# Kernel optimization log

Hardware: AMD Instinct MI355X
Metric: run time of the kernel (lower is better)

Reference implementation:

```python
import jax, jax.numpy as jnp
import numpy as np

K = 12
CHUNK = 1024
N_LAYERS = 4
WIDTH = 192
COND = 64
PE_DIM = 3 * 8 * 2 + 3  # 51
OUT_SCALE = 0.01
BIG = 1e9


def _build_knn(x, k=K, chunk=CHUNK):
    """Brute-force kNN, row-chunked like the TF double-chunked version.
    x: (N,3) float32 -> (N,k) int32 neighbor indices (self excluded)."""
    n = x.shape[0]
    x = x.astype(jnp.float32)
    x_sq = jnp.sum(x * x, axis=1)  # (N,)
    col_ids = jnp.arange(n, dtype=jnp.int32)
    starts = jnp.arange(0, n, chunk, dtype=jnp.int32)

    def one_chunk(start):
        xc = jax.lax.dynamic_slice(x, (start, 0), (chunk, 3))        # (chunk,3)
        sq_c = jax.lax.dynamic_slice(x_sq, (start,), (chunk,))       # (chunk,)
        d = sq_c[:, None] + x_sq[None, :] - 2.0 * (xc @ x.T)         # (chunk,N)
        d = jnp.maximum(d, 0.0)
        rows = start + jnp.arange(chunk, dtype=jnp.int32)
        d = d + jnp.where(rows[:, None] == col_ids[None, :], BIG, 0.0)  # exclude self
        _, idx = jax.lax.top_k(-d, k)                                 # smallest distances
        return idx.astype(jnp.int32)

    idx = jax.lax.map(one_chunk, starts)  # (n/chunk, chunk, k)
    return idx.reshape(n, k)


def _fourier(x, Bs):
    """concat_k [sin(xB_k), cos(xB_k)] + x  -> (N, PE_DIM)."""
    feats = []
    for B in Bs:
        xb = x @ B  # (N,8)
        feats.append(jnp.sin(xb))
        feats.append(jnp.cos(xb))
    feats.append(x)
    return jnp.concatenate(feats, axis=-1)


def setup_inputs() -> dict:
    key = jax.random.key(0)
    ks = jax.random.split(key, 16)
    n = 32768
    x = jax.random.normal(ks[0], (n, 3), dtype=jnp.float32)
    z = jax.random.normal(ks[1], (COND,), dtype=jnp.float32)
    sigmas = (1.0, 10.0, 50.0)
    B0 = jax.random.normal(ks[2], (3, 8), dtype=jnp.float32) * sigmas[0]
    B1 = jax.random.normal(ks[3], (3, 8), dtype=jnp.float32) * sigmas[1]
    B2 = jax.random.normal(ks[4], (3, 8), dtype=jnp.float32) * sigmas[2]
    in_total = PE_DIM + COND  # 115
    s = 0.05
    Wp = jax.random.normal(ks[5], (in_total, WIDTH), dtype=jnp.float32) * s
    bp = jnp.zeros((WIDTH,), dtype=jnp.float32)
    mix_dim = WIDTH + WIDTH + 6  # feat + agg + rel_feat
    Wl = jax.random.normal(ks[6], (N_LAYERS, mix_dim, WIDTH), dtype=jnp.float32) * s
    bl = jnp.zeros((N_LAYERS, WIDTH), dtype=jnp.float32)
    # FiLM: kernel ~zeros, gamma bias=ones, beta bias=zeros (perturbed slightly)
    Wg = jax.random.normal(ks[7], (N_LAYERS, COND, WIDTH), dtype=jnp.float32) * 0.01
    bg = jnp.ones((N_LAYERS, WIDTH), dtype=jnp.float32)
    Wb = jax.random.normal(ks[8], (N_LAYERS, COND, WIDTH), dtype=jnp.float32) * 0.01
    bb = jnp.zeros((N_LAYERS, WIDTH), dtype=jnp.float32)
    Wout = jax.random.normal(ks[9], (WIDTH, 3), dtype=jnp.float32) * s
    bout = jnp.zeros((3,), dtype=jnp.float32)
    return {"x": x, "z": z, "B0": B0, "B1": B1, "B2": B2,
            "Wp": Wp, "bp": bp, "Wl": Wl, "bl": bl,
            "Wg": Wg, "bg": bg, "Wb": Wb, "bb": bb,
            "Wout": Wout, "bout": bout}


def reference(x, z, B0, B1, B2, Wp, bp, Wl, bl, Wg, bg, Wb, bb, Wout, bout):
    n = x.shape[0]
    knn_idx = _build_knn(x)                     # (N,K) int32
    pe = _fourier(x, (B0, B1, B2))              # (N,51)
    zb = jnp.broadcast_to(z[None, :], (n, COND))
    feat = jnp.concatenate([pe, zb], axis=-1)   # (N,115)
    h = jax.nn.silu(feat @ Wp + bp)             # (N,WIDTH)
    # precompute relative-coordinate stats (same for all layers)
    nbr_coords = x[knn_idx]                     # (N,K,3)
    rel = nbr_coords - x[:, None, :]
    rel_feat = jnp.concatenate([rel.mean(axis=1), rel.std(axis=1)], axis=-1)  # (N,6)
    for li in range(N_LAYERS):
        nbr = h[knn_idx]                        # (N,K,WIDTH) gather
        agg = nbr.mean(axis=1)                  # (N,WIDTH)
        mix = jnp.concatenate([h, agg, rel_feat], axis=-1)  # (N,390)
        h = jax.nn.silu(mix @ Wl[li] + bl[li])
        gamma = z @ Wg[li] + bg[li]             # (WIDTH,)
        beta = z @ Wb[li] + bb[li]
        h = h * gamma[None, :] + beta[None, :]  # FiLM
    out = (h @ Wout + bout) * OUT_SCALE         # (N,3)
    return out
```

## Files before the change

### kernel.cpp

```cpp
#include <hip/hip_runtime.h>
#include <math.h>

#define WIDTH 192
#define KNN 12
#define G 64
#define NCELLS (G * G * G)
#define SMAX 8

#define CE(a, b) { double _lo = fmin(a, b); double _hi = fmax(a, b); a = _lo; b = _hi; }
#define INSERT12(key) { \
    b11 = fmin(b11, key); \
    CE(b10, b11); CE(b9, b10); CE(b8, b9); CE(b7, b8); CE(b6, b7); \
    CE(b5, b6);  CE(b4, b5); CE(b3, b4); CE(b2, b3); CE(b1, b2); CE(b0, b1); }
#define DECL12 double b0,b1,b2,b3,b4,b5,b6,b7,b8,b9,b10,b11
#define INIT12 { b0=__hiloint2double(0x7F7FFFFF,0);  b1=__hiloint2double(0x7F7FFFFF,1); \
    b2=__hiloint2double(0x7F7FFFFF,2);  b3=__hiloint2double(0x7F7FFFFF,3); \
    b4=__hiloint2double(0x7F7FFFFF,4);  b5=__hiloint2double(0x7F7FFFFF,5); \
    b6=__hiloint2double(0x7F7FFFFF,6);  b7=__hiloint2double(0x7F7FFFFF,7); \
    b8=__hiloint2double(0x7F7FFFFF,8);  b9=__hiloint2double(0x7F7FFFFF,9); \
    b10=__hiloint2double(0x7F7FFFFF,10); b11=__hiloint2double(0x7F7FFFFF,11); }

#define MERGE_STAGE(m) { \
    double pb11 = shflx_d(b11, m), pb10 = shflx_d(b10, m), pb9 = shflx_d(b9, m); \
    double pb8  = shflx_d(b8, m),  pb7  = shflx_d(b7, m),  pb6 = shflx_d(b6, m); \
    double pb5  = shflx_d(b5, m),  pb4  = shflx_d(b4, m),  pb3 = shflx_d(b3, m); \
    double pb2  = shflx_d(b2, m),  pb1  = shflx_d(b1, m),  pb0 = shflx_d(b0, m); \
    double c12 = pb3, c13 = pb2, c14 = pb1, c15 = pb0; \
    b4 = fmin(b4, pb11); b5 = fmin(b5, pb10); b6 = fmin(b6, pb9);  b7 = fmin(b7, pb8); \
    b8 = fmin(b8, pb7);  b9 = fmin(b9, pb6);  b10 = fmin(b10, pb5); b11 = fmin(b11, pb4); \
    CE(b0, b8);  CE(b1, b9);  CE(b2, b10); CE(b3, b11); \
    CE(b4, c12); CE(b5, c13); CE(b6, c14); CE(b7, c15); \
    CE(b0, b4);  CE(b1, b5);  CE(b2, b6);  CE(b3, b7); \
    CE(b8, c12); CE(b9, c13); CE(b10, c14); CE(b11, c15); \
    CE(b0, b2);  CE(b1, b3);  CE(b4, b6);  CE(b5, b7); \
    CE(b8, b10); CE(b9, b11); \
    CE(b0, b1);  CE(b2, b3);  CE(b4, b5);  CE(b6, b7); \
    CE(b8, b9);  CE(b10, b11); }

__device__ inline unsigned encf(float f) {
    unsigned u = __float_as_uint(f);
    return (u & 0x80000000u) ? ~u : (u | 0x80000000u);
}
__device__ inline float decf(unsigned u) {
    return (u & 0x80000000u) ? __uint_as_float(u & 0x7fffffffu) : __uint_as_float(~u);
}
__device__ inline int cellc(float v, float mn, float invh) {
    int c = (int)((v - mn) * invh);
    return min(max(c, 0), G - 1);
}
__device__ inline double shflx_d(double v, int m) {
    int lo = __shfl_xor(__double2loint(v), m, 64);
    int hi = __shfl_xor(__double2hiint(v), m, 64);
    return __hiloint2double(hi, lo);
}

__device__ inline float wave_union_d12(
    double b0, double b1, double b2, double b3, double b4, double b5,
    double b6, double b7, double b8, double b9, double b10, double b11)
{
#pragma unroll
    for (int m = 1; m <= 32; m <<= 1) MERGE_STAGE(m)
    return __int_as_float(__double2hiint(b11));
}

__global__ __launch_bounds__(256) void prep_kernel(
    const float4* __restrict__ sorted, const float* __restrict__ B0,
    const float* __restrict__ B1, const float* __restrict__ B2,
    float* __restrict__ pe, int n)
{
    int i = blockIdx.x * 256 + threadIdx.x;
    float4 q = sorted[i];
    float x0 = q.x, x1 = q.y, x2 = q.z;
    const float* Bm[3] = {B0, B1, B2};
    float* pr = pe + (size_t)i * 64;
#pragma unroll
    for (int m = 0; m < 3; ++m) {
        const float* B = Bm[m];
#pragma unroll
        for (int k = 0; k < 8; ++k) {
            float arg = x0 * B[k] + x1 * B[8 + k] + x2 * B[16 + k];
            pr[m * 16 + k]     = sinf(arg);
            pr[m * 16 + 8 + k] = cosf(arg);
        }
    }
    pr[48] = x0; pr[49] = x1; pr[50] = x2;
#pragma unroll
    for (int c = 51; c < 64; ++c) pr[c] = 0.0f;
}

__global__ __launch_bounds__(256) void precompute_kernel(
    const float* __restrict__ z, const float* __restrict__ Wp, const float* __restrict__ bp,
    const float* __restrict__ Wg, const float* __restrict__ bg,
    const float* __restrict__ Wb, const float* __restrict__ bb,
    float* __restrict__ bias0, float* __restrict__ gammaB, float* __restrict__ betaB)
{
    __shared__ float zs[64];
    int t = threadIdx.x;
    if (t < 64) zs[t] = z[t];
    __syncthreads();
    if (t < WIDTH) {
        float acc = bp[t];
        for (int k = 0; k < 64; ++k) acc += zs[k] * Wp[(51 + k) * WIDTH + t];
        bias0[t] = acc;
        for (int l = 0; l < 4; ++l) {
            float g = bg[l * WIDTH + t];
            float b = bb[l * WIDTH + t];
            for (int k = 0; k < 64; ++k) {
                g += zs[k] * Wg[(l * 64 + k) * WIDTH + t];
                b += zs[k] * Wb[(l * 64 + k) * WIDTH + t];
            }
            gammaB[l * WIDTH + t] = g;
            betaB[l * WIDTH + t] = b;
        }
    }
}

__global__ __launch_bounds__(64) void init_bbox_kernel(unsigned* __restrict__ bb)
{
    int t = threadIdx.x;
    if (t < 3) bb[t] = 0xFFFFFFFFu;
    else if (t < 6) bb[t] = 0u;
}

__global__ __launch_bounds__(256) void bbox_kernel(
    const float* __restrict__ x, unsigned* __restrict__ bb, int n)
{
    int i = blockIdx.x * 256 + threadIdx.x;
    unsigned emin[3], emax[3];
#pragma unroll
    for (int a = 0; a < 3; ++a) { unsigned e = encf(x[i * 3 + a]); emin[a] = e; emax[a] = e; }
#pragma unroll
    for (int o = 32; o; o >>= 1) {
#pragma unroll
        for (int a = 0; a < 3; ++a) {
            emin[a] = min(emin[a], (unsigned)__shfl_xor((int)emin[a], o, 64));
            emax[a] = max(emax[a], (unsigned)__shfl_xor((int)emax[a], o, 64));
        }
    }
    if ((threadIdx.x & 63) == 0) {
#pragma unroll
        for (int a = 0; a < 3; ++a) {
            atomicMin(&bb[a], emin[a]);
            atomicMax(&bb[3 + a], emax[a]);
        }
    }
}

__global__ __launch_bounds__(256) void hist_kernel(
    const float* __restrict__ x, const unsigned* __restrict__ bb,
    unsigned* __restrict__ counts, unsigned long long* __restrict__ rowmask, int n)
{
    int i = blockIdx.x * 256 + threadIdx.x;
    float mnx = decf(bb[0]), mny = decf(bb[1]), mnz = decf(bb[2]);
    float ivx = (float)G / (decf(bb[3]) - mnx);
    float ivy = (float)G / (decf(bb[4]) - mny);
    float ivz = (float)G / (decf(bb[5]) - mnz);
    int cx = cellc(x[i * 3 + 0], mnx, ivx);
    int cy = cellc(x[i * 3 + 1], mny, ivy);
    int cz = cellc(x[i * 3 + 2], mnz, ivz);
    atomicAdd(&counts[(cz * G + cy) * G + cx], 1u);
    atomicOr(&rowmask[cz * G + cy], 1ull << cx);
}

__global__ __launch_bounds__(256) void scan1_kernel(
    const unsigned* __restrict__ counts, unsigned* __restrict__ offs,
    unsigned* __restrict__ bsums)
{
    __shared__ unsigned s[256];
    int b = blockIdx.x, t = threadIdx.x;
    unsigned base = (unsigned)b * 1024 + t * 4;
    unsigned v[4], sum = 0;
#pragma unroll
    for (int k = 0; k < 4; ++k) { v[k] = counts[base + k]; sum += v[k]; }
    s[t] = sum; __syncthreads();
    for (int off = 1; off < 256; off <<= 1) {
        unsigned xv = (t >= off) ? s[t - off] : 0u;
        __syncthreads();
        s[t] += xv;
        __syncthreads();
    }
    unsigned excl = s[t] - sum;
    if (t == 255) bsums[b] = s[255];
    unsigned run = excl;
#pragma unroll
    for (int k = 0; k < 4; ++k) { offs[base + k] = run; run += v[k]; }
}

__global__ __launch_bounds__(256) void scan2_kernel(unsigned* __restrict__ bsums)
{
    __shared__ unsigned s[256];
    int t = threadIdx.x;
    unsigned v = bsums[t];
    s[t] = v; __syncthreads();
    for (int off = 1; off < 256; off <<= 1) {
        unsigned xv = (t >= off) ? s[t - off] : 0u;
        __syncthreads();
        s[t] += xv;
        __syncthreads();
    }
    bsums[t] = s[t] - v;
}

__global__ __launch_bounds__(256) void scan3_kernel(
    unsigned* __restrict__ offs, const unsigned* __restrict__ bsums,
    unsigned* __restrict__ cursors, int n)
{
    int b = blockIdx.x, t = threadIdx.x;
    unsigned add = bsums[b];
    unsigned base = (unsigned)b * 1024 + t * 4;
#pragma unroll
    for (int k = 0; k < 4; ++k) {
        unsigned v = offs[base + k] + add;
        offs[base + k] = v;
        cursors[base + k] = v;
    }
    if (b == 255 && t == 255) offs[NCELLS] = (unsigned)n;
}

__global__ __launch_bounds__(256) void scatter_kernel(
    const float* __restrict__ x, const unsigned* __restrict__ bb,
    unsigned* __restrict__ cursors, float4* __restrict__ sorted,
    unsigned* __restrict__ inv, int n)
{
    int i = blockIdx.x * 256 + threadIdx.x;
    float mnx = decf(bb[0]), mny = decf(bb[1]), mnz = decf(bb[2]);
    float ivx = (float)G / (decf(bb[3]) - mnx);
    float ivy = (float)G / (decf(bb[4]) - mny);
    float ivz = (float)G / (decf(bb[5]) - mnz);
    float x0 = x[i * 3 + 0], x1 = x[i * 3 + 1], x2 = x[i * 3 + 2];
    int cx = cellc(x0, mnx, ivx);
    int cy = cellc(x1, mny, ivy);
    int cz = cellc(x2, mnz, ivz);
    unsigned pos = atomicAdd(&cursors[(cz * G + cy) * G + cx], 1u);
    sorted[pos] = make_float4(x0, x1, x2, __int_as_float(i));
    inv[i] = pos;
}

__global__ __launch_bounds__(256) void knn_grid_kernel(
    const float4* __restrict__ sorted, const unsigned* __restrict__ offs,
    const unsigned long long* __restrict__ rowmask,
    const unsigned* __restrict__ bb, const float* __restrict__ x,
    const unsigned* __restrict__ inv,
    unsigned short* __restrict__ knn, float* __restrict__ relf, int n)
{
    const int tid = threadIdx.x;
    const int l = tid & 63;
    const int nb = gridDim.x;
    const int b = blockIdx.x;
    const int fb = (b & 1) ? (nb - 1 - (b >> 1)) : (b >> 1);
    const int p = fb * 4 + (tid >> 6);

    float mnx = decf(bb[0]), mny = decf(bb[1]), mnz = decf(bb[2]);
    float mxx = decf(bb[3]), mxy = decf(bb[4]), mxz = decf(bb[5]);
    float hx = (mxx - mnx) / G, hy = (mxy - mny) / G, hz = (mxz - mnz) / G;
    float ivx = (float)G / (mxx - mnx);
    float ivy = (float)G / (mxy - mny);
    float ivz = (float)G / (mxz - mnz);

    float4 q = sorted[p];
    float xi = q.x, yi = q.y, zi = q.z;
    int iorig = __float_as_int(q.w);
    float sqi = fmaf(zi, zi, fmaf(yi, yi, xi * xi));
    int cx = cellc(xi, mnx, ivx), cy = cellc(yi, mny, ivy), cz = cellc(zi, mnz, ivz);
    float fx = (xi - mnx) - cx * hx;
    float fy = (yi - mny) - cy * hy;
    float fz = (zi - mnz) - cz * hz;

    DECL12; INIT12;
    float worst = 3.402823466e+38f;
    float worst_g = 3.402823466e+38f;

    auto waveMinWorst = [&]() -> float {
        float wm = worst;
        wm = fminf(wm, __shfl_xor(wm, 1, 64));
        wm = fminf(wm, __shfl_xor(wm, 2, 64));
        wm = fminf(wm, __shfl_xor(wm, 4, 64));
        wm = fminf(wm, __shfl_xor(wm, 8, 64));
        wm = fminf(wm, __shfl_xor(wm, 16, 64));
        wm = fminf(wm, __shfl_xor(wm, 32, 64));
        return wm;
    };

    auto lane12Bound = [&]() -> float {
        float v = __int_as_float(__double2hiint(b0));
#pragma unroll
        for (int k = 2; k <= 64; k <<= 1) {
#pragma unroll
            for (int j = k >> 1; j >= 1; j >>= 1) {
                float pv = __shfl_xor(v, j, 64);
                bool dir = ((l & k) == 0);
                bool lower = ((l & j) == 0);
                float mn = fminf(v, pv), mx = fmaxf(v, pv);
                v = (lower == dir) ? mn : mx;
            }
        }
        return __shfl(v, 11, 64);
    };

    auto scanRange = [&](int c0, int c1) {
        unsigned j0 = offs[c0], j1 = offs[c1 + 1];
        if (j0 >= j1) return;
        float4 c = sorted[j0];
        for (unsigned t = j0; t < j1; ++t) {
            unsigned tn = (t + 1 < j1) ? t + 1 : t;
            float4 nx = sorted[tn];
            float sqj = fmaf(c.z, c.z, fmaf(c.y, c.y, c.x * c.x));
            float dot = fmaf(zi, c.z, fmaf(yi, c.y, xi * c.x));
            float d = fmaf(-2.0f, dot, sqi + sqj);
            int jg = __float_as_int(c.w);
            if (d <= fminf(worst, worst_g) && jg != iorig) {
                d = fmaxf(d, 0.0f);
                double key = __hiloint2double(__float_as_int(d), jg);
                INSERT12(key);
                worst = __int_as_float(__double2hiint(b11));
            }
            c = nx;
        }
    };

    bool done = false;
    for (int s = 0; s <= SMAX; ++s) {
        if (s > 0) {
            float bx = (s - 1) * hx + fminf(fx, hx - fx);
            float by = (s - 1) * hy + fminf(fy, hy - fy);
            float bz = (s - 1) * hz + fminf(fz, hz - fz);
            float bnd = fminf(bx, fminf(by, bz));
            float bnd2 = bnd * bnd;
            worst_g = fminf(worst_g, waveMinWorst());
            if (bnd2 > worst_g + 1e-4f) { done = true; break; }
            worst_g = fminf(worst_g, lane12Bound());
            if (bnd2 > worst_g + 1e-4f) { done = true; break; }
            if (s >= 4) {
                worst_g = fminf(worst_g,
                    wave_union_d12(b0,b1,b2,b3,b4,b5,b6,b7,b8,b9,b10,b11));
                if (bnd2 > worst_g + 1e-4f) { done = true; break; }
            }
        }
        if (s == 0) {
            if (l == 0) {
                int row = cz * G + cy;
                if ((rowmask[row] >> cx) & 1ull) {
                    int rb = row * G;
                    scanRange(rb + cx, rb + cx);
                }
            }
        } else {
            int w2 = 2 * s + 1;
            float rcp = 1.0f / (float)w2;
            int nrows = w2 * w2;
            for (int r = l; r < nrows; r += 64) {
                int qd = (int)((float)r * rcp);
                int rem = r - qd * w2;
                if (rem < 0) { qd--; rem += w2; }
                else if (rem >= w2) { qd++; rem -= w2; }
                int dz = qd - s, dy = rem - s;
                int zz = cz + dz, yy = cy + dy;
                if (zz < 0 || zz >= G || yy < 0 || yy >= G) continue;
                int row = zz * G + yy;
                unsigned long long rm = rowmask[row];
                if (rm == 0ull) continue;
                int rb = row * G;
                int adz = dz < 0 ? -dz : dz, ady = dy < 0 ? -dy : dy;
                if (adz == s || ady == s) {
                    int x0 = max(cx - s, 0), x1 = min(cx + s, G - 1);
                    unsigned long long msk =
                        ((x1 == 63) ? ~0ull : ((1ull << (x1 + 1)) - 1ull)) &
                        ~((1ull << x0) - 1ull);
                    unsigned long long mm = rm & msk;
                    if (mm) {
                        int c0 = __ffsll((unsigned long long)mm) - 1;
                        int c1 = 63 - __clzll((long long)mm);
                        scanRange(rb + c0, rb + c1);
                    }
                } else {
                    int xm = cx - s, xp = cx + s;
                    if (xm >= 0 && ((rm >> xm) & 1ull)) scanRange(rb + xm, rb + xm);
                    if (xp < G  && ((rm >> xp) & 1ull)) scanRange(rb + xp, rb + xp);
                }
            }
        }
    }
    if (!done) {
        float bx = SMAX * hx + fminf(fx, hx - fx);
        float by = SMAX * hy + fminf(fy, hy - fy);
        float bz = SMAX * hz + fminf(fz, hz - fz);
        float bnd = fminf(bx, fminf(by, bz));
        float bnd2 = bnd * bnd;
        worst_g = fminf(worst_g, waveMinWorst());
        if (bnd2 > worst_g + 1e-4f) done = true;
        if (!done) {
            worst_g = fminf(worst_g, lane12Bound());
            if (bnd2 > worst_g + 1e-4f) done = true;
        }
        if (!done) {
            worst_g = fminf(worst_g,
                wave_union_d12(b0,b1,b2,b3,b4,b5,b6,b7,b8,b9,b10,b11));
            if (bnd2 > worst_g + 1e-4f) done = true;
        }
    }
    if (!done) {
        INIT12;
        worst = 3.402823466e+38f; worst_g = 3.402823466e+38f;
        for (int base = 0; base < n; base += 512) {
            float4 cc[8];
#pragma unroll
            for (int r = 0; r < 8; ++r) cc[r] = sorted[base + l + r * 64];
#pragma unroll
            for (int r = 0; r < 8; ++r) {
                float4 c = cc[r];
                float sqj = fmaf(c.z, c.z, fmaf(c.y, c.y, c.x * c.x));
                float dot = fmaf(zi, c.z, fmaf(yi, c.y, xi * c.x));
                float d = fmaf(-2.0f, dot, sqi + sqj);
                int jg = __float_as_int(c.w);
                if (d <= fminf(worst, worst_g) && jg != iorig) {
                    d = fmaxf(d, 0.0f);
                    double key = __hiloint2double(__float_as_int(d), jg);
                    INSERT12(key);
                    worst = __int_as_float(__double2hiint(b11));
                }
            }
            worst_g = fminf(worst_g, waveMinWorst());
        }
    }

#pragma unroll
    for (int m = 1; m <= 32; m <<= 1) MERGE_STAGE(m)

    if (l == 0) {
        int idx[KNN];
        idx[0]=__double2loint(b0);  idx[1]=__double2loint(b1);  idx[2]=__double2loint(b2);
        idx[3]=__double2loint(b3);  idx[4]=__double2loint(b4);  idx[5]=__double2loint(b5);
        idx[6]=__double2loint(b6);  idx[7]=__double2loint(b7);  idx[8]=__double2loint(b8);
        idx[9]=__double2loint(b9);  idx[10]=__double2loint(b10); idx[11]=__double2loint(b11);

        float rx[KNN], ry[KNN], rz[KNN];
        float sx = 0.f, sy = 0.f, sz = 0.f;
#pragma unroll
        for (int s = 0; s < KNN; ++s) {
            int j = idx[s];
            knn[(size_t)p * KNN + s] = (unsigned short)inv[j];
            rx[s] = x[(size_t)j * 3 + 0] - xi;
            ry[s] = x[(size_t)j * 3 + 1] - yi;
            rz[s] = x[(size_t)j * 3 + 2] - zi;
            sx += rx[s]; sy += ry[s]; sz += rz[s];
        }
        float mx = sx / 12.0f, my = sy / 12.0f, mz = sz / 12.0f;
        float vx = 0.f, vy = 0.f, vz = 0.f;
#pragma unroll
        for (int s = 0; s < KNN; ++s) {
            float dx = rx[s] - mx, dy = ry[s] - my, dz = rz[s] - mz;
            vx += dx * dx; vy += dy * dy; vz += dz * dz;
        }
        float* rr = relf + (size_t)p * 8;
        rr[0] = mx; rr[1] = my; rr[2] = mz;
        rr[3] = sqrtf(vx / 12.0f); rr[4] = sqrtf(vy / 12.0f); rr[5] = sqrtf(vz / 12.0f);
        rr[6] = 0.0f; rr[7] = 0.0f;
    }
}

template <bool LAYER>
__global__ __launch_bounds__(256) void gemm_silu_kernel(
    const float* __restrict__ A0, const float* __restrict__ Agg,
    const float* __restrict__ Rel,
    const float* __restrict__ W, const float* __restrict__ bias,
    const float* __restrict__ gamma, const float* __restrict__ beta,
    float* __restrict__ out)
{
    __shared__ float As[16][68];
    __shared__ float Bs[16][196];
    const int tid = threadIdx.x;
    const int ty = tid >> 4, tx = tid & 15;
    const int m0 = blockIdx.x * 64;
    const int arow = tid >> 2, akoff = (tid & 3) * 4;
    const int bk = tid >> 4,  bc = (tid & 15) * 12;

    float acc[4][12] = {};
    const int NCH = LAYER ? 24 : 4;

    auto loadA = [&](int ch) -> float4 {
        int k0 = ch * 16;
        const float* src; int stride, col;
        if (!LAYER)            { src = A0;  stride = 64;  col = k0 + akoff; }
        else if (k0 < 192)     { src = A0;  stride = 192; col = k0 + akoff; }
        else                   { src = Agg; stride = 192; col = k0 - 192 + akoff; }
        return *(const float4*)&src[(size_t)(m0 + arow) * stride + col];
    };

    float4 ra = loadA(0);
    const float* wr0 = &W[(size_t)bk * 192 + bc];
    float4 rb0 = *(const float4*)&wr0[0];
    float4 rb1 = *(const float4*)&wr0[4];
    float4 rb2 = *(const float4*)&wr0[8];

    for (int ch = 0; ch < NCH; ++ch) {
        As[akoff + 0][arow] = ra.x; As[akoff + 1][arow] = ra.y;
        As[akoff + 2][arow] = ra.z; As[akoff + 3][arow] = ra.w;
        *(float4*)&Bs[bk][bc + 0] = rb0;
        *(float4*)&Bs[bk][bc + 4] = rb1;
        *(float4*)&Bs[bk][bc + 8] = rb2;
        __syncthreads();
        if (ch + 1 < NCH) {
            ra = loadA(ch + 1);
            const float* wr = &W[(size_t)((ch + 1) * 16 + bk) * 192 + bc];
            rb0 = *(const float4*)&wr[0];
            rb1 = *(const float4*)&wr[4];
            rb2 = *(const float4*)&wr[8];
        }
#pragma unroll
        for (int k = 0; k < 16; ++k) {
            float4 a0 = *(const float4*)&As[k][ty * 4];
            float av[4] = {a0.x, a0.y, a0.z, a0.w};
            float4 q0 = *(const float4*)&Bs[k][tx * 12 + 0];
            float4 q1 = *(const float4*)&Bs[k][tx * 12 + 4];
            float4 q2 = *(const float4*)&Bs[k][tx * 12 + 8];
            float bv[12] = {q0.x, q0.y, q0.z, q0.w, q1.x, q1.y, q1.z, q1.w,
                            q2.x, q2.y, q2.z, q2.w};
#pragma unroll
            for (int a = 0; a < 4; ++a)
#pragma unroll
                for (int b = 0; b < 12; ++b)
                    acc[a][b] = fmaf(av[a], bv[b], acc[a][b]);
        }
        __syncthreads();
    }

    if (LAYER) {
        {
            int row = tid >> 2, cp = (tid & 3) * 2;
            float2 v = *(const float2*)&Rel[(size_t)(m0 + row) * 8 + cp];
            As[cp + 0][row] = v.x; As[cp + 1][row] = v.y;
        }
        {
            int k2 = tid >> 4, c = (tid & 15) * 12;
            if (k2 < 8) {
                int gk = 384 + k2; if (gk > 389) gk = 389;
                const float* wr = &W[(size_t)gk * 192 + c];
                *(float4*)&Bs[k2][c + 0] = *(const float4*)&wr[0];
                *(float4*)&Bs[k2][c + 4] = *(const float4*)&wr[4];
                *(float4*)&Bs[k2][c + 8] = *(const float4*)&wr[8];
            }
        }
        __syncthreads();
#pragma unroll
        for (int k = 0; k < 8; ++k) {
            float4 a0 = *(const float4*)&As[k][ty * 4];
            float av[4] = {a0.x, a0.y, a0.z, a0.w};
            float4 q0 = *(const float4*)&Bs[k][tx * 12 + 0];
            float4 q1 = *(const float4*)&Bs[k][tx * 12 + 4];
            float4 q2 = *(const float4*)&Bs[k][tx * 12 + 8];
            float bv[12] = {q0.x, q0.y, q0.z, q0.w, q1.x, q1.y, q1.z, q1.w,
                            q2.x, q2.y, q2.z, q2.w};
#pragma unroll
            for (int a = 0; a < 4; ++a)
#pragma unroll
                for (int b = 0; b < 12; ++b)
                    acc[a][b] = fmaf(av[a], bv[b], acc[a][b]);
        }
        __syncthreads();
    }

#pragma unroll
    for (int a = 0; a < 4; ++a) {
        int gi = m0 + ty * 4 + a;
        float res[12];
#pragma unroll
        for (int b = 0; b < 12; ++b) {
            int gc = tx * 12 + b;
            float v = acc[a][b] + bias[gc];
            float s = 1.0f / (1.0f + expf(-v));
            v = v * s;
            if (LAYER) v = v * gamma[gc] + beta[gc];
            res[b] = v;
        }
        float* orow = &out[(size_t)gi * 192 + tx * 12];
        *(float4*)&orow[0] = make_float4(res[0], res[1], res[2], res[3]);
        *(float4*)&orow[4] = make_float4(res[4], res[5], res[6], res[7]);
        *(float4*)&orow[8] = make_float4(res[8], res[9], res[10], res[11]);
    }
}

__global__ __launch_bounds__(256) void agg_kernel(
    const float4* __restrict__ h4, const unsigned short* __restrict__ knn,
    float4* __restrict__ agg4, int n)
{
    int flat = blockIdx.x * 256 + threadIdx.x;
    int i = flat / 48;
    int c4 = flat - i * 48;
    const unsigned short* kn = knn + (size_t)i * KNN;
    float4 s = make_float4(0.f, 0.f, 0.f, 0.f);
#pragma unroll
    for (int j = 0; j < KNN; ++j) {
        float4 v = h4[(size_t)kn[j] * 48 + c4];
        s.x += v.x; s.y += v.y; s.z += v.z; s.w += v.w;
    }
    const float r = 1.0f / 12.0f;
    agg4[flat] = make_float4(s.x * r, s.y * r, s.z * r, s.w * r);
}

__global__ __launch_bounds__(256) void out_kernel(
    const float4* __restrict__ h4, const float4* __restrict__ sorted,
    const float* __restrict__ Wout, const float* __restrict__ bout,
    float* __restrict__ out, int n)
{
    __shared__ float w[576];
    int t = threadIdx.x;
    for (int e = t; e < 576; e += 256) w[e] = Wout[e];
    __syncthreads();
    int i = blockIdx.x * 256 + t;
    float a0 = 0.f, a1 = 0.f, a2 = 0.f;
    for (int k4 = 0; k4 < 48; ++k4) {
        float4 hv = h4[(size_t)i * 48 + k4];
        int k = k4 * 4;
        a0 = fmaf(hv.x, w[k * 3 + 0], a0); a1 = fmaf(hv.x, w[k * 3 + 1], a1); a2 = fmaf(hv.x, w[k * 3 + 2], a2);
        a0 = fmaf(hv.y, w[k * 3 + 3], a0); a1 = fmaf(hv.y, w[k * 3 + 4], a1); a2 = fmaf(hv.y, w[k * 3 + 5], a2);
        a0 = fmaf(hv.z, w[k * 3 + 6], a0); a1 = fmaf(hv.z, w[k * 3 + 7], a1); a2 = fmaf(hv.z, w[k * 3 + 8], a2);
        a0 = fmaf(hv.w, w[k * 3 + 9], a0); a1 = fmaf(hv.w, w[k * 3 + 10], a1); a2 = fmaf(hv.w, w[k * 3 + 11], a2);
    }
    int iorig = __float_as_int(sorted[i].w);
    out[(size_t)iorig * 3 + 0] = (a0 + bout[0]) * 0.01f;
    out[(size_t)iorig * 3 + 1] = (a1 + bout[1]) * 0.01f;
    out[(size_t)iorig * 3 + 2] = (a2 + bout[2]) * 0.01f;
}

extern "C" void kernel_launch(void* const* d_in, const int* in_sizes, int n_in,
                              void* d_out, int out_size, void* d_ws, size_t ws_size,
                              hipStream_t stream)
{
    const float* x    = (const float*)d_in[0];
    const float* z    = (const float*)d_in[1];
    const float* B0   = (const float*)d_in[2];
    const float* B1   = (const float*)d_in[3];
    const float* B2   = (const float*)d_in[4];
    const float* Wp   = (const float*)d_in[5];
    const float* bp   = (const float*)d_in[6];
    const float* Wl   = (const float*)d_in[7];
    const float* bl   = (const float*)d_in[8];
    const float* Wg   = (const float*)d_in[9];
    const float* bg   = (const float*)d_in[10];
    const float* Wb   = (const float*)d_in[11];
    const float* bb   = (const float*)d_in[12];
    const float* Wout = (const float*)d_in[13];
    const float* bout = (const float*)d_in[14];

    int n = in_sizes[0] / 3;

    float* ws = (float*)d_ws;
    float* bias0  = ws;
    float* gammaB = ws + 192;
    float* betaB  = ws + 960;
    size_t off = 1728;
    unsigned short* knn = (unsigned short*)(ws + off);  off += (size_t)n * 6;
    float* relf = ws + off;                off += (size_t)n * 8;
    float4* sorted = (float4*)(ws + off);  off += (size_t)n * 4;
    float* hA   = ws + off;                off += (size_t)n * 192;
    float* hB   = ws + off;                off += (size_t)n * 192;
    float* aggb = ws + off;                off += (size_t)n * 192;

    unsigned* bbx     = (unsigned*)hA;
    unsigned* counts  = bbx + 8;
    unsigned* offsA   = counts + NCELLS;
    unsigned* cursors = offsA + NCELLS + 1;
    unsigned* bsums   = cursors + NCELLS;
    size_t gu = 8 + (size_t)NCELLS * 3 + 1 + 256;
    gu = (gu + 1) & ~(size_t)1;
    unsigned long long* rowmask = (unsigned long long*)((unsigned*)hA + gu);
    gu += (size_t)G * G * 2;
    unsigned* inv = (unsigned*)hA + gu;
    float* pe = hB;

    init_bbox_kernel<<<1, 64, 0, stream>>>(bbx);
    hipMemsetAsync(counts, 0, (size_t)NCELLS * 4, stream);
    hipMemsetAsync(rowmask, 0, (size_t)G * G * 8, stream);
    precompute_kernel<<<1, 256, 0, stream>>>(z, Wp, bp, Wg, bg, Wb, bb,
                                             bias0, gammaB, betaB);
    bbox_kernel<<<n / 256, 256, 0, stream>>>(x, bbx, n);
    hist_kernel<<<n / 256, 256, 0, stream>>>(x, bbx, counts, rowmask, n);
    scan1_kernel<<<NCELLS / 1024, 256, 0, stream>>>(counts, offsA, bsums);
    scan2_kernel<<<1, 256, 0, stream>>>(bsums);
    scan3_kernel<<<NCELLS / 1024, 256, 0, stream>>>(offsA, bsums, cursors, n);
    scatter_kernel<<<n / 256, 256, 0, stream>>>(x, bbx, cursors, sorted, inv, n);
    prep_kernel<<<n / 256, 256, 0, stream>>>(sorted, B0, B1, B2, pe, n);
    knn_grid_kernel<<<n / 4, 256, 0, stream>>>(sorted, offsA, rowmask, bbx, x,
                                               inv, knn, relf, n);

    gemm_silu_kernel<false><<<n / 64, 256, 0, stream>>>(
        pe, nullptr, nullptr, Wp, bias0, nullptr, nullptr, hA);

    float* hcur = hA;
    float* hnxt = hB;
    for (int li = 0; li < 4; ++li) {
        agg_kernel<<<(size_t)n * 48 / 256, 256, 0, stream>>>(
            (const float4*)hcur, knn, (float4*)aggb, n);
        gemm_silu_kernel<true><<<n / 64, 256, 0, stream>>>(
            hcur, aggb, relf,
            Wl + (size_t)li * 390 * 192, bl + (size_t)li * 192,
            gammaB + (size_t)li * 192, betaB + (size_t)li * 192, hnxt);
        float* t = hcur; hcur = hnxt; hnxt = t;
    }

    out_kernel<<<n / 256, 256, 0, stream>>>((const float4*)hcur, sorted,
                                            Wout, bout, (float*)d_out, n);
}
```

Baseline: 846.1 us.

## Widen GEMM per-thread tile to 8x12 with 128 threads; parallelize center-cell kNN scan

The SiLU GEMM kernel now runs 128 threads per block, and each thread computes an 8x12 output tile instead of 4x12. Each thread loads twice as much of the A and W tiles per chunk. This raises register reuse and FMA density per shared-memory load, at the cost of more registers and fewer threads per block. Separately, the kNN center-cell scan is spread across all 64 lanes with a strided loop instead of running on lane 0 alone, which removes a serial hotspot.

```diff
diff --git a/kernel.cpp b/kernel.cpp
--- a/kernel.cpp
+++ b/kernel.cpp
@@ -318,6 +318,23 @@
         }
     };
 
+    auto scanRangeStrided = [&](int c0, int c1) {
+        unsigned j0 = offs[c0], j1 = offs[c1 + 1];
+        for (unsigned t = j0 + l; t < j1; t += 64) {
+            float4 c = sorted[t];
+            float sqj = fmaf(c.z, c.z, fmaf(c.y, c.y, c.x * c.x));
+            float dot = fmaf(zi, c.z, fmaf(yi, c.y, xi * c.x));
+            float d = fmaf(-2.0f, dot, sqi + sqj);
+            int jg = __float_as_int(c.w);
+            if (d <= fminf(worst, worst_g) && jg != iorig) {
+                d = fmaxf(d, 0.0f);
+                double key = __hiloint2double(__float_as_int(d), jg);
+                INSERT12(key);
+                worst = __int_as_float(__double2hiint(b11));
+            }
+        }
+    };
+
     bool done = false;
     for (int s = 0; s <= SMAX; ++s) {
         if (s > 0) {
@@ -337,12 +354,10 @@
             }
         }
         if (s == 0) {
-            if (l == 0) {
-                int row = cz * G + cy;
-                if ((rowmask[row] >> cx) & 1ull) {
-                    int rb = row * G;
-                    scanRange(rb + cx, rb + cx);
-                }
+            int row = cz * G + cy;
+            if ((rowmask[row] >> cx) & 1ull) {
+                int rb = row * G;
+                scanRangeStrided(rb + cx, rb + cx);
             }
         } else {
             int w2 = 2 * s + 1;
@@ -459,7 +474,7 @@
 }
 
 template <bool LAYER>
-__global__ __launch_bounds__(256) void gemm_silu_kernel(
+__global__ __launch_bounds__(128) void gemm_silu_kernel(
     const float* __restrict__ A0, const float* __restrict__ Agg,
     const float* __restrict__ Rel,
     const float* __restrict__ W, const float* __restrict__ bias,
@@ -471,13 +486,13 @@
     const int tid = threadIdx.x;
     const int ty = tid >> 4, tx = tid & 15;
     const int m0 = blockIdx.x * 64;
-    const int arow = tid >> 2, akoff = (tid & 3) * 4;
+    const int arow = tid >> 1, akoff = (tid & 1) * 8;
     const int bk = tid >> 4,  bc = (tid & 15) * 12;
 
-    float acc[4][12] = {};
+    float acc[8][12] = {};
     const int NCH = LAYER ? 24 : 4;
 
-    auto loadA = [&](int ch) -> float4 {
+    auto loadA0 = [&](int ch) -> float4 {
         int k0 = ch * 16;
         const float* src; int stride, col;
         if (!LAYER)            { src = A0;  stride = 64;  col = k0 + akoff; }
@@ -485,92 +500,106 @@
         else                   { src = Agg; stride = 192; col = k0 - 192 + akoff; }
         return *(const float4*)&src[(size_t)(m0 + arow) * stride + col];
     };
-
-    float4 ra = loadA(0);
-    const float* wr0 = &W[(size_t)bk * 192 + bc];
-    float4 rb0 = *(const float4*)&wr0[0];
-    float4 rb1 = *(const float4*)&wr0[4];
-    float4 rb2 = *(const float4*)&wr0[8];
+    auto loadA1 = [&](int ch) -> float4 {
+        int k0 = ch * 16;
+        const float* src; int stride, col;
+        if (!LAYER)            { src = A0;  stride = 64;  col = k0 + akoff + 4; }
+        else if (k0 < 192)     { src = A0;  stride = 192; col = k0 + akoff + 4; }
+        else                   { src = Agg; stride = 192; col = k0 - 192 + akoff + 4; }
+        return *(const float4*)&src[(size_t)(m0 + arow) * stride + col];
+    };
+
+    float4 ra0 = loadA0(0), ra1 = loadA1(0);
+    const float* w0 = &W[(size_t)bk * 192 + bc];
+    const float* w1 = &W[(size_t)(bk + 8) * 192 + bc];
+    float4 rb0 = *(const float4*)&w0[0], rb1 = *(const float4*)&w0[4], rb2 = *(const float4*)&w0[8];
+    float4 rb3 = *(const float4*)&w1[0], rb4 = *(const float4*)&w1[4], rb5 = *(const float4*)&w1[8];
 
     for (int ch = 0; ch < NCH; ++ch) {
-        As[akoff + 0][arow] = ra.x; As[akoff + 1][arow] = ra.y;
-        As[akoff + 2][arow] = ra.z; As[akoff + 3][arow] = ra.w;
+        As[akoff + 0][arow] = ra0.x; As[akoff + 1][arow] = ra0.y;
+        As[akoff + 2][arow] = ra0.z; As[akoff + 3][arow] = ra0.w;
+        As[akoff + 4][arow] = ra1.x; As[akoff + 5][arow] = ra1.y;
+        As[akoff + 6][arow] = ra1.z; As[akoff + 7][arow] = ra1.w;
         *(float4*)&Bs[bk][bc + 0] = rb0;
         *(float4*)&Bs[bk][bc + 4] = rb1;
         *(float4*)&Bs[bk][bc + 8] = rb2;
+        *(float4*)&Bs[bk + 8][bc + 0] = rb3;
+        *(float4*)&Bs[bk + 8][bc + 4] = rb4;
+        *(float4*)&Bs[bk + 8][bc + 8] = rb5;
         __syncthreads();
         if (ch + 1 < NCH) {
-            ra = loadA(ch + 1);
-            const float* wr = &W[(size_t)((ch + 1) * 16 + bk) * 192 + bc];
-            rb0 = *(const float4*)&wr[0];
-            rb1 = *(const float4*)&wr[4];
-            rb2 = *(const float4*)&wr[8];
+            ra0 = loadA0(ch + 1); ra1 = loadA1(ch + 1);
+            const float* wn0 = &W[(size_t)((ch + 1) * 16 + bk) * 192 + bc];
+            const float* wn1 = &W[(size_t)((ch + 1) * 16 + bk + 8) * 192 + bc];
+            rb0 = *(const float4*)&wn0[0]; rb1 = *(const float4*)&wn0[4]; rb2 = *(const float4*)&wn0[8];
+            rb3 = *(const float4*)&wn1[0]; rb4 = *(const float4*)&wn1[4]; rb5 = *(const float4*)&wn1[8];
         }
 #pragma unroll
         for (int k = 0; k < 16; ++k) {
-            float4 a0 = *(const float4*)&As[k][ty * 4];
-            float av[4] = {a0.x, a0.y, a0.z, a0.w};
+            float4 a0 = *(const float4*)&As[k][ty * 8 + 0];
+            float4 a1 = *(const float4*)&As[k][ty * 8 + 4];
+            float av[8] = {a0.x, a0.y, a0.z, a0.w, a1.x, a1.y, a1.z, a1.w};
             float4 q0 = *(const float4*)&Bs[k][tx * 12 + 0];
             float4 q1 = *(const float4*)&Bs[k][tx * 12 + 4];
             float4 q2 = *(const float4*)&Bs[k][tx * 12 + 8];
             float bv[12] = {q0.x, q0.y, q0.z, q0.w, q1.x, q1.y, q1.z, q1.w,
                             q2.x, q2.y, q2.z, q2.w};
 #pragma unroll
-            for (int a = 0; a < 4; ++a)
-#pragma unroll
-                for (int b = 0; b < 12; ++b)
-                    acc[a][b] = fmaf(av[a], bv[b], acc[a][b]);
+            for (int a = 0; a < 8; ++a)
+#pragma unroll
+                for (int bcol = 0; bcol < 12; ++bcol)
+                    acc[a][bcol] = fmaf(av[a], bv[bcol], acc[a][bcol]);
         }
         __syncthreads();
     }
 
     if (LAYER) {
         {
-            int row = tid >> 2, cp = (tid & 3) * 2;
-            float2 v = *(const float2*)&Rel[(size_t)(m0 + row) * 8 + cp];
+            int row = tid >> 1, cp = (tid & 1) * 4;
+            float4 v = *(const float4*)&Rel[(size_t)(m0 + row) * 8 + cp];
             As[cp + 0][row] = v.x; As[cp + 1][row] = v.y;
+            As[cp + 2][row] = v.z; As[cp + 3][row] = v.w;
         }
         {
             int k2 = tid >> 4, c = (tid & 15) * 12;
-            if (k2 < 8) {
-                int gk = 384 + k2; if (gk > 389) gk = 389;
-                const float* wr = &W[(size_t)gk * 192 + c];
-                *(float4*)&Bs[k2][c + 0] = *(const float4*)&wr[0];
-                *(float4*)&Bs[k2][c + 4] = *(const float4*)&wr[4];
-                *(float4*)&Bs[k2][c + 8] = *(const float4*)&wr[8];
-            }
+            int gk = 384 + k2; if (gk > 389) gk = 389;
+            const float* wr = &W[(size_t)gk * 192 + c];
+            *(float4*)&Bs[k2][c + 0] = *(const float4*)&wr[0];
+            *(float4*)&Bs[k2][c + 4] = *(const float4*)&wr[4];
+            *(float4*)&Bs[k2][c + 8] = *(const float4*)&wr[8];
         }
         __syncthreads();
 #pragma unroll
         for (int k = 0; k < 8; ++k) {
-            float4 a0 = *(const float4*)&As[k][ty * 4];
-            float av[4] = {a0.x, a0.y, a0.z, a0.w};
+            float4 a0 = *(const float4*)&As[k][ty * 8 + 0];
+            float4 a1 = *(const float4*)&As[k][ty * 8 + 4];
+            float av[8] = {a0.x, a0.y, a0.z, a0.w, a1.x, a1.y, a1.z, a1.w};
             float4 q0 = *(const float4*)&Bs[k][tx * 12 + 0];
             float4 q1 = *(const float4*)&Bs[k][tx * 12 + 4];
             float4 q2 = *(const float4*)&Bs[k][tx * 12 + 8];
             float bv[12] = {q0.x, q0.y, q0.z, q0.w, q1.x, q1.y, q1.z, q1.w,
                             q2.x, q2.y, q2.z, q2.w};
 #pragma unroll
-            for (int a = 0; a < 4; ++a)
-#pragma unroll
-                for (int b = 0; b < 12; ++b)
-                    acc[a][b] = fmaf(av[a], bv[b], acc[a][b]);
+            for (int a = 0; a < 8; ++a)
+#pragma unroll
+                for (int bcol = 0; bcol < 12; ++bcol)
+                    acc[a][bcol] = fmaf(av[a], bv[bcol], acc[a][bcol]);
         }
         __syncthreads();
     }
 
 #pragma unroll
-    for (int a = 0; a < 4; ++a) {
-        int gi = m0 + ty * 4 + a;
+    for (int a = 0; a < 8; ++a) {
+        int gi = m0 + ty * 8 + a;
         float res[12];
 #pragma unroll
-        for (int b = 0; b < 12; ++b) {
-            int gc = tx * 12 + b;
-            float v = acc[a][b] + bias[gc];
+        for (int bcol = 0; bcol < 12; ++bcol) {
+            int gc = tx * 12 + bcol;
+            float v = acc[a][bcol] + bias[gc];
             float s = 1.0f / (1.0f + expf(-v));
             v = v * s;
             if (LAYER) v = v * gamma[gc] + beta[gc];
-            res[b] = v;
+            res[bcol] = v;
         }
         float* orow = &out[(size_t)gi * 192 + tx * 12];
         *(float4*)&orow[0] = make_float4(res[0], res[1], res[2], res[3]);
@@ -683,7 +712,7 @@
     knn_grid_kernel<<<n / 4, 256, 0, stream>>>(sorted, offsA, rowmask, bbx, x,
                                                inv, knn, relf, n);
 
-    gemm_silu_kernel<false><<<n / 64, 256, 0, stream>>>(
+    gemm_silu_kernel<false><<<n / 64, 128, 0, stream>>>(
         pe, nullptr, nullptr, Wp, bias0, nullptr, nullptr, hA);
 
     float* hcur = hA;
@@ -691,7 +720,7 @@
     for (int li = 0; li < 4; ++li) {
         agg_kernel<<<(size_t)n * 48 / 256, 256, 0, stream>>>(
             (const float4*)hcur, knn, (float4*)aggb, n);
-        gemm_silu_kernel<true><<<n / 64, 256, 0, stream>>>(
+        gemm_silu_kernel<true><<<n / 64, 128, 0, stream>>>(
             hcur, aggb, relf,
             Wl + (size_t)li * 390 * 192, bl + (size_t)li * 192,
             gammaB + (size_t)li * 192, betaB + (size_t)li * 192, hnxt);
```

Result: slower. 877.3 us (+3.7%).

## Double-buffer GEMM shared tiles and stride center-cell kNN scan across lanes

Applied to the files above, without the earlier changes.

The GEMM kernel now ping-pongs between two shared-memory buffers for the A and B tiles, dropping the trailing barrier from each k-chunk so one sync per iteration remains. The kNN search's initial own-cell scan is spread across all 64 lanes with a strided loop instead of running on lane 0 alone, so per-lane candidate lists are filled in parallel. Double buffering doubles shared-memory use per block, which may reduce occupancy. The strided scan relies on the later wave-level merge to combine per-lane results.

```diff
diff --git a/kernel.cpp b/kernel.cpp
--- a/kernel.cpp
+++ b/kernel.cpp
@@ -318,6 +318,23 @@
         }
     };
 
+    auto scanRangeStrided = [&](int c0, int c1) {
+        unsigned j0 = offs[c0], j1 = offs[c1 + 1];
+        for (unsigned t = j0 + l; t < j1; t += 64) {
+            float4 c = sorted[t];
+            float sqj = fmaf(c.z, c.z, fmaf(c.y, c.y, c.x * c.x));
+            float dot = fmaf(zi, c.z, fmaf(yi, c.y, xi * c.x));
+            float d = fmaf(-2.0f, dot, sqi + sqj);
+            int jg = __float_as_int(c.w);
+            if (d <= fminf(worst, worst_g) && jg != iorig) {
+                d = fmaxf(d, 0.0f);
+                double key = __hiloint2double(__float_as_int(d), jg);
+                INSERT12(key);
+                worst = __int_as_float(__double2hiint(b11));
+            }
+        }
+    };
+
     bool done = false;
     for (int s = 0; s <= SMAX; ++s) {
         if (s > 0) {
@@ -337,12 +354,10 @@
             }
         }
         if (s == 0) {
-            if (l == 0) {
-                int row = cz * G + cy;
-                if ((rowmask[row] >> cx) & 1ull) {
-                    int rb = row * G;
-                    scanRange(rb + cx, rb + cx);
-                }
+            int row = cz * G + cy;
+            if ((rowmask[row] >> cx) & 1ull) {
+                int rb = row * G;
+                scanRangeStrided(rb + cx, rb + cx);
             }
         } else {
             int w2 = 2 * s + 1;
@@ -466,8 +481,8 @@
     const float* __restrict__ gamma, const float* __restrict__ beta,
     float* __restrict__ out)
 {
-    __shared__ float As[16][68];
-    __shared__ float Bs[16][196];
+    __shared__ float As[2][16][68];
+    __shared__ float Bs[2][16][196];
     const int tid = threadIdx.x;
     const int ty = tid >> 4, tx = tid & 15;
     const int m0 = blockIdx.x * 64;
@@ -493,11 +508,12 @@
     float4 rb2 = *(const float4*)&wr0[8];
 
     for (int ch = 0; ch < NCH; ++ch) {
-        As[akoff + 0][arow] = ra.x; As[akoff + 1][arow] = ra.y;
-        As[akoff + 2][arow] = ra.z; As[akoff + 3][arow] = ra.w;
-        *(float4*)&Bs[bk][bc + 0] = rb0;
-        *(float4*)&Bs[bk][bc + 4] = rb1;
-        *(float4*)&Bs[bk][bc + 8] = rb2;
+        const int buf = ch & 1;
+        As[buf][akoff + 0][arow] = ra.x; As[buf][akoff + 1][arow] = ra.y;
+        As[buf][akoff + 2][arow] = ra.z; As[buf][akoff + 3][arow] = ra.w;
+        *(float4*)&Bs[buf][bk][bc + 0] = rb0;
+        *(float4*)&Bs[buf][bk][bc + 4] = rb1;
+        *(float4*)&Bs[buf][bk][bc + 8] = rb2;
         __syncthreads();
         if (ch + 1 < NCH) {
             ra = loadA(ch + 1);
@@ -508,53 +524,54 @@
         }
 #pragma unroll
         for (int k = 0; k < 16; ++k) {
-            float4 a0 = *(const float4*)&As[k][ty * 4];
+            float4 a0 = *(const float4*)&As[buf][k][ty * 4];
             float av[4] = {a0.x, a0.y, a0.z, a0.w};
-            float4 q0 = *(const float4*)&Bs[k][tx * 12 + 0];
-            float4 q1 = *(const float4*)&Bs[k][tx * 12 + 4];
-            float4 q2 = *(const float4*)&Bs[k][tx * 12 + 8];
+            float4 q0 = *(const float4*)&Bs[buf][k][tx * 12 + 0];
+            float4 q1 = *(const float4*)&Bs[buf][k][tx * 12 + 4];
+            float4 q2 = *(const float4*)&Bs[buf][k][tx * 12 + 8];
             float bv[12] = {q0.x, q0.y, q0.z, q0.w, q1.x, q1.y, q1.z, q1.w,
                             q2.x, q2.y, q2.z, q2.w};
 #pragma unroll
             for (int a = 0; a < 4; ++a)
 #pragma unroll
-                for (int b = 0; b < 12; ++b)
-                    acc[a][b] = fmaf(av[a], bv[b], acc[a][b]);
-        }
-        __syncthreads();
-    }
+                for (int bcol = 0; bcol < 12; ++bcol)
+                    acc[a][bcol] = fmaf(av[a], bv[bcol], acc[a][bcol]);
+        }
+    }
+    __syncthreads();
 
     if (LAYER) {
+        const int buf = NCH & 1;
         {
             int row = tid >> 2, cp = (tid & 3) * 2;
             float2 v = *(const float2*)&Rel[(size_t)(m0 + row) * 8 + cp];
-            As[cp + 0][row] = v.x; As[cp + 1][row] = v.y;
+            As[buf][cp + 0][row] = v.x; As[buf][cp + 1][row] = v.y;
         }
         {
             int k2 = tid >> 4, c = (tid & 15) * 12;
             if (k2 < 8) {
                 int gk = 384 + k2; if (gk > 389) gk = 389;
                 const float* wr = &W[(size_t)gk * 192 + c];
-                *(float4*)&Bs[k2][c + 0] = *(const float4*)&wr[0];
-                *(float4*)&Bs[k2][c + 4] = *(const float4*)&wr[4];
-                *(float4*)&Bs[k2][c + 8] = *(const float4*)&wr[8];
+                *(float4*)&Bs[buf][k2][c + 0] = *(const float4*)&wr[0];
+                *(float4*)&Bs[buf][k2][c + 4] = *(const float4*)&wr[4];
+                *(float4*)&Bs[buf][k2][c + 8] = *(const float4*)&wr[8];
             }
         }
         __syncthreads();
 #pragma unroll
         for (int k = 0; k < 8; ++k) {
-            float4 a0 = *(const float4*)&As[k][ty * 4];
+            float4 a0 = *(const float4*)&As[buf][k][ty * 4];
             float av[4] = {a0.x, a0.y, a0.z, a0.w};
-            float4 q0 = *(const float4*)&Bs[k][tx * 12 + 0];
-            float4 q1 = *(const float4*)&Bs[k][tx * 12 + 4];
-            float4 q2 = *(const float4*)&Bs[k][tx * 12 + 8];
+            float4 q0 = *(const float4*)&Bs[buf][k][tx * 12 + 0];
+            float4 q1 = *(const float4*)&Bs[buf][k][tx * 12 + 4];
+            float4 q2 = *(const float4*)&Bs[buf][k][tx * 12 + 8];
             float bv[12] = {q0.x, q0.y, q0.z, q0.w, q1.x, q1.y, q1.z, q1.w,
                             q2.x, q2.y, q2.z, q2.w};
 #pragma unroll
             for (int a = 0; a < 4; ++a)
 #pragma unroll
-                for (int b = 0; b < 12; ++b)
-                    acc[a][b] = fmaf(av[a], bv[b], acc[a][b]);
+                for (int bcol = 0; bcol < 12; ++bcol)
+                    acc[a][bcol] = fmaf(av[a], bv[bcol], acc[a][bcol]);
         }
         __syncthreads();
     }
@@ -564,13 +581,13 @@
         int gi = m0 + ty * 4 + a;
         float res[12];
 #pragma unroll
-        for (int b = 0; b < 12; ++b) {
-            int gc = tx * 12 + b;
-            float v = acc[a][b] + bias[gc];
+        for (int bcol = 0; bcol < 12; ++bcol) {
+            int gc = tx * 12 + bcol;
+            float v = acc[a][bcol] + bias[gc];
             float s = 1.0f / (1.0f + expf(-v));
             v = v * s;
             if (LAYER) v = v * gamma[gc] + beta[gc];
-            res[b] = v;
+            res[bcol] = v;
         }
         float* orow = &out[(size_t)gi * 192 + tx * 12];
         *(float4*)&orow[0] = make_float4(res[0], res[1], res[2], res[3]);
```

Result: slower. 884.6 us (+4.5%).
